# Kernel optimization log

Hardware: AMD Instinct MI355X
Metric: run time of the kernel (lower is better)

## Reference

```python
import jax, jax.numpy as jnp
import numpy as np

FILTER_LENGTH = 1024
HOP_LENGTH = 512
CUTOFF = FILTER_LENGTH // 2 + 1  # 513


def make_forward_basis():
    # fourier_basis = fft(eye(N)); stack [real(top half); imag(top half)]
    fb = np.fft.fft(np.eye(FILTER_LENGTH))
    fb = np.vstack([np.real(fb[:CUTOFF, :]), np.imag(fb[:CUTOFF, :])]).astype(np.float32)
    return jnp.asarray(fb)  # [2*CUTOFF, FILTER_LENGTH] = [1026, 1024]


def setup_inputs() -> dict:
    key = jax.random.key(0)
    input_data = jax.random.normal(key, (64, 524288), dtype=jnp.float32)
    return {"input_data": input_data, "forward_basis": make_forward_basis()}


def reference(input_data, forward_basis):
    # input_data: [B, T] -> [B, 1, T]
    x = input_data[:, None, :]
    # forward_basis: [1026, 1024] -> conv kernel [out_ch=1026, in_ch=1, K=1024]
    w = forward_basis[:, None, :]
    # F.conv1d(..., stride=hop, padding=filter_length)
    ft = jax.lax.conv_general_dilated(
        x, w,
        window_strides=(HOP_LENGTH,),
        padding=[(FILTER_LENGTH, FILTER_LENGTH)],
    )  # [B, 1026, frames]
    real_part = ft[:, :CUTOFF, :]
    imag_part = ft[:, CUTOFF:, :]
    magnitude = jnp.sqrt(real_part ** 2 + imag_part ** 2 + 1e-10)
    phase = jnp.arctan2(imag_part, real_part)
    return magnitude, phase
```

## Files before the change

kernel.cpp:

```cpp
#include <hip/hip_runtime.h>
#include <math.h>

#define BATCH 64
#define LSAMP 524288
#define KLEN 1024
#define HOP 512
#define CBIN 513
#define TWIN 1027
#define BCT (64LL * 513 * 1027)

typedef unsigned int uint32;
using short8  = __attribute__((ext_vector_type(8))) short;
using ushort8v= __attribute__((ext_vector_type(8))) unsigned short;
using f32x4   = __attribute__((ext_vector_type(4))) float;

#define FBT_SLOTS (9 * 32 * 512)
#define FBH_OFF 0u
#define FBL_OFF ((uint32)FBT_SLOTS * 8u)
#define XPLANE  526336
#define XH_OFF  (2u * (uint32)FBT_SLOTS * 8u)
#define XL_OFF  (XH_OFF + 64u * (uint32)XPLANE)
#define WS_NEED ((size_t)(XL_OFF + 64u * (uint32)XPLANE) * 2)

__device__ __forceinline__ unsigned short bfh(float v) {
    uint32 u = __float_as_uint(v);
    return (unsigned short)((u + 0x7fffu + ((u >> 16) & 1u)) >> 16);
}
__device__ __forceinline__ float bf2f(unsigned short h) {
    return __uint_as_float(((uint32)h) << 16);
}

__device__ __forceinline__ void gld16(const void* g, void* l) {
    using GT = const __attribute__((address_space(1))) unsigned int;
    using LT = __attribute__((address_space(3))) unsigned int;
    __builtin_amdgcn_global_load_lds((GT*)g, (LT*)l, 16, 0, 0);
}

__global__ __launch_bounds__(256)
void split_fb(const float* __restrict__ fb, unsigned short* __restrict__ ws) {
    int id = blockIdx.x * 256 + threadIdx.x;
    if (id >= FBT_SLOTS) return;
    int slot = id & 511;
    int tile = id >> 9;
    int ks = tile & 31;
    int ct = tile >> 5;
    int row = slot >> 2;
    int unit = (slot & 3) ^ ((row >> 1) & 3);
    int c0 = (ct < 8) ? ct * 64 : 449;
    int c = (row < 64) ? (c0 + row) : (513 + c0 + (row - 64));
    int k0 = ks * 32 + unit * 8;
    const float4* src = (const float4*)(fb + (size_t)c * KLEN + k0);
    float4 a = src[0], b = src[1];
    float vv[8] = {a.x, a.y, a.z, a.w, b.x, b.y, b.z, b.w};
    ushort8v hh, ll;
#pragma unroll
    for (int j = 0; j < 8; ++j) {
        unsigned short h = bfh(vv[j]);
        hh[j] = h;
        ll[j] = bfh(vv[j] - bf2f(h));
    }
    *(ushort8v*)&ws[FBH_OFF + (size_t)id * 8] = hh;
    *(ushort8v*)&ws[FBL_OFF + (size_t)id * 8] = ll;
}

__global__ __launch_bounds__(256)
void split_x(const float* __restrict__ x, unsigned short* __restrict__ ws) {
    long i = (long)blockIdx.x * 256 + threadIdx.x;
    if (i >= 64L * (XPLANE / 8)) return;
    int b = (int)(i / (XPLANE / 8));
    int j = (int)(i % (XPLANE / 8)) * 8;
    long sample = (long)j - 1024;
    float vv[8] = {0.f,0.f,0.f,0.f,0.f,0.f,0.f,0.f};
    if (sample >= 0 && sample < LSAMP) {
        const float4* s = (const float4*)(x + (size_t)b * LSAMP + sample);
        float4 a = s[0], c = s[1];
        vv[0]=a.x; vv[1]=a.y; vv[2]=a.z; vv[3]=a.w;
        vv[4]=c.x; vv[5]=c.y; vv[6]=c.z; vv[7]=c.w;
    }
    ushort8v hh, ll;
#pragma unroll
    for (int jj = 0; jj < 8; ++jj) {
        unsigned short h = bfh(vv[jj]);
        hh[jj] = h;
        ll[jj] = bfh(vv[jj] - bf2f(h));
    }
    *(ushort8v*)&ws[(size_t)XH_OFF + (size_t)b * XPLANE + j] = hh;
    *(ushort8v*)&ws[(size_t)XL_OFF + (size_t)b * XPLANE + j] = ll;
}

__global__ __launch_bounds__(256, 2)
void stft_gemm(const unsigned short* __restrict__ ws, float* __restrict__ out) {
    extern __shared__ unsigned short sm[];

    const int tid  = threadIdx.x;
    const int lane = tid & 63;
    const int w    = tid >> 6;
    const int wm   = w >> 1;
    const int wn   = w & 1;
    const int lm   = lane & 15;
    const int lg   = lane >> 4;
    const int swz  = (lm >> 1) & 3;

    const int p   = blockIdx.x;
    const int xcd = p & 7;
    const int q   = p >> 3;
    const int ct  = q % 9;
    const int g   = (q / 9) * 8 + xcd;
    const int nt  = g % 9;
    const int b   = g / 9;
    const int c0  = (ct < 8) ? ct * 64 : 449;
    const int n0  = nt * 128;

    f32x4 acc[4][4];
#pragma unroll
    for (int i = 0; i < 4; ++i)
#pragma unroll
        for (int j = 0; j < 4; ++j) acc[i][j] = (f32x4)0.f;

    auto STAGE = [&](int d, int ks) {
        const int s0 = w * 128;
        const uint32 atile = (uint32)(ct * 32 + ks) * 4096u;
#pragma unroll
        for (int r = 0; r < 2; ++r) {
            const int sbase = s0 + r * 64;
            const uint32 slot = (uint32)(sbase + lane);
            const uint32 dsto = (uint32)d * 16384u + (uint32)sbase * 8u;
            gld16(&ws[atile + slot * 8u],            &sm[dsto]);
            gld16(&ws[FBL_OFF + atile + slot * 8u],  &sm[dsto + 4096u]);
            const uint32 brow  = slot >> 2;
            const uint32 bunit = (slot & 3u) ^ ((brow >> 1) & 3u);
            uint32 pidx = (uint32)(n0 + brow) * 512u + (uint32)ks * 32u + bunit * 8u;
            if (pidx > (uint32)(XPLANE - 8)) pidx = (uint32)(XPLANE - 8);
            gld16(&ws[(size_t)XH_OFF + (size_t)b * XPLANE + pidx], &sm[dsto + 8192u]);
            gld16(&ws[(size_t)XL_OFF + (size_t)b * XPLANE + pidx], &sm[dsto + 12288u]);
        }
    };

    STAGE(0, 0);
    __syncthreads();

    for (int ks = 0; ks < 32; ++ks) {
        const int cur = ks & 1;
        if (ks < 31) STAGE(cur ^ 1, ks + 1);

        const uint32 base = (uint32)cur * 16384u;
        short8 ah[4], al[4], bh[4], bl[4];
#pragma unroll
        for (int mi = 0; mi < 4; ++mi) {
            const uint32 row = (uint32)(wm * 64 + mi * 16 + lm);
            const uint32 o = base + row * 32u + (uint32)((lg ^ swz) * 8);
            ah[mi] = *(const short8*)&sm[o];
            al[mi] = *(const short8*)&sm[o + 4096u];
        }
#pragma unroll
        for (int ni = 0; ni < 4; ++ni) {
            const uint32 row = (uint32)(wn * 64 + ni * 16 + lm);
            const uint32 o = base + 8192u + row * 32u + (uint32)((lg ^ swz) * 8);
            bh[ni] = *(const short8*)&sm[o];
            bl[ni] = *(const short8*)&sm[o + 4096u];
        }
#pragma unroll
        for (int mi = 0; mi < 4; ++mi)
#pragma unroll
            for (int ni = 0; ni < 4; ++ni)
                acc[mi][ni] = __builtin_amdgcn_mfma_f32_16x16x32_bf16(ah[mi], bh[ni], acc[mi][ni], 0, 0, 0);
#pragma unroll
        for (int mi = 0; mi < 4; ++mi)
#pragma unroll
            for (int ni = 0; ni < 4; ++ni)
                acc[mi][ni] = __builtin_amdgcn_mfma_f32_16x16x32_bf16(ah[mi], bl[ni], acc[mi][ni], 0, 0, 0);
#pragma unroll
        for (int mi = 0; mi < 4; ++mi)
#pragma unroll
            for (int ni = 0; ni < 4; ++ni)
                acc[mi][ni] = __builtin_amdgcn_mfma_f32_16x16x32_bf16(al[mi], bh[ni], acc[mi][ni], 0, 0, 0);

        __syncthreads();
    }

    float* eps = (float*)sm;
#pragma unroll
    for (int mi = 0; mi < 4; ++mi)
#pragma unroll
        for (int ni = 0; ni < 4; ++ni)
#pragma unroll
            for (int r = 0; r < 4; ++r) {
                int cr = mi * 16 + lg * 4 + r;
                int nc = wn * 64 + ni * 16 + lm;
                eps[wm * 8448 + cr * 132 + nc] = acc[mi][ni][r];
            }
    __syncthreads();
#pragma unroll 4
    for (int qq = 0; qq < 32; ++qq) {
        int id = qq * 256 + tid;
        int cr = id >> 7, nc = id & 127;
        int n = n0 + nc;
        if (n < TWIN) {
            float re = eps[cr * 132 + nc];
            float im = eps[8448 + cr * 132 + nc];
            size_t obase = ((size_t)b * CBIN + (c0 + cr)) * TWIN + n;
            out[obase]       = sqrtf(fmaf(re, re, fmaf(im, im, 1e-10f)));
            out[BCT + obase] = atan2f(im, re);
        }
    }
}

__global__ __launch_bounds__(256)
void stft_fix(const float* __restrict__ x, const float* __restrict__ fb,
              float* __restrict__ out) {
    const int lane = threadIdx.x & 63;
    const uint32 nquad = (uint32)(BCT / 4);
    const uint32 nquad_pad = (nquad + 63u) & ~63u;
    const uint32 stride = gridDim.x * 256;
    for (uint32 gq = blockIdx.x * 256 + threadIdx.x; gq < nquad_pad; gq += stride) {
        const bool live = gq < nquad;
        float mm[4] = {1e9f, 1e9f, 1e9f, 1e9f};
        float pp[4] = {0.f, 0.f, 0.f, 0.f};
        if (live) {
            float4 mv = *(const float4*)&out[(size_t)gq * 4];
            float4 pv = *(const float4*)&out[BCT + (size_t)gq * 4];
            mm[0]=mv.x; mm[1]=mv.y; mm[2]=mv.z; mm[3]=mv.w;
            pp[0]=pv.x; pp[1]=pv.y; pp[2]=pv.z; pp[3]=pv.w;
        }
        bool cand = false;
#pragma unroll
        for (int j = 0; j < 4; ++j)
            cand |= (mm[j] < 2e-3f) || ((3.14159265f - fabsf(pp[j])) * mm[j] < 3e-3f);
        if (__ballot(cand) == 0ULL) continue;

        bool risky[4] = {false, false, false, false};
        if (live) {
            uint32 i0  = gq * 4u;
            uint32 row = i0 / 1027u;
            uint32 t0  = i0 - row * 1027u;
            uint32 cc0 = row % 513u;
#pragma unroll
            for (int j = 0; j < 4; ++j) {
                uint32 t = t0 + j, c = cc0;
                if (t >= 1027u) { t -= 1027u; c = (c == 512u) ? 0u : c + 1u; }
                bool edge = (t == 0u) | (t == 1026u);
                bool axis = (c == 0u) | (c == 512u);
                risky[j] = !edge && ((mm[j] < 2e-3f) ||
                                     (!axis && (3.14159265f - fabsf(pp[j])) * mm[j] < 3e-3f));
            }
        }
#pragma unroll
        for (int j = 0; j < 4; ++j) {
            unsigned long long mask = __ballot(risky[j]);
            while (mask) {
                int src = __ffsll(mask) - 1;
                mask &= mask - 1;
                uint32 idx = (gq - lane + (uint32)src) * 4u + (uint32)j;
                uint32 rw = idx / 1027u;
                uint32 t  = idx - rw * 1027u;
                uint32 bb = rw / 513u;
                uint32 c  = rw - bb * 513u;
                const float* xb = x + (size_t)bb * LSAMP;
                const float* fr = fb + (size_t)c * KLEN;
                const float* fi = fb + (size_t)(513 + c) * KLEN;
                const long s = (long)t * HOP - KLEN;
                double re = 0.0, im = 0.0;
                for (int k = lane; k < KLEN; k += 64) {
                    long gg = s + k;
                    double xv = (gg >= 0 && gg < LSAMP) ? (double)xb[gg] : 0.0;
                    re = fma((double)fr[k], xv, re);
                    im = fma((double)fi[k], xv, im);
                }
#pragma unroll
                for (int off = 32; off > 0; off >>= 1) {
                    re += __shfl_down(re, off);
                    im += __shfl_down(im, off);
                }
                if (lane == 0) {
                    out[idx]       = (float)sqrt(re * re + im * im + 1e-10);
                    out[BCT + idx] = (float)atan2(im, re);
                }
            }
        }
    }
}

__global__ __launch_bounds__(256)
void stft_gemm_legacy(const float* __restrict__ x, const float* __restrict__ fb,
                      float* __restrict__ out) {
    __shared__ unsigned short sml[16384];
    unsigned short* AH = sml;
    unsigned short* AL = sml + 4096;
    unsigned short* BH = sml + 8192;
    unsigned short* BL = sml + 12288;

    const int tid  = threadIdx.x;
    const int lane = tid & 63;
    const int w    = tid >> 6;
    const int wm   = w >> 1;
    const int wn   = w & 1;
    const int lm   = lane & 15;
    const int lk   = (lane >> 4) * 8;

    const int ct = blockIdx.x;
    const int nt = blockIdx.y;
    const int b  = blockIdx.z;
    const int c0 = ct * 64;
    const int n0 = nt * 128;

    const float4* fbg = (const float4*)fb;
    const float*  xb  = x + (size_t)b * LSAMP;

    int srow[4], su[4], sfbrow[4];
    long sxbase0[4];
#pragma unroll
    for (int pp = 0; pp < 4; ++pp) {
        int id = pp * 256 + tid;
        int row = id >> 3, u = id & 7;
        srow[pp] = row; su[pp] = u;
        sfbrow[pp] = (row < 64) ? (c0 + row) : (513 + c0 + (row - 64));
        sxbase0[pp] = 512L * (n0 + row) + 4L * u - 1024L;
    }

    f32x4 acc[4][4];
#pragma unroll
    for (int i = 0; i < 4; ++i)
#pragma unroll
        for (int j = 0; j < 4; ++j) acc[i][j] = (f32x4)0.f;

    float4 pa[4], pb[4];
#pragma unroll
    for (int pp = 0; pp < 4; ++pp) {
        pa[pp] = fbg[(size_t)sfbrow[pp] * 256 + su[pp]];
        long base = sxbase0[pp];
        pb[pp] = (base >= 0 && base < LSAMP) ? *(const float4*)(xb + base)
                                             : make_float4(0.f, 0.f, 0.f, 0.f);
    }

    for (int ks = 0; ks < 32; ++ks) {
        __syncthreads();
#pragma unroll
        for (int pp = 0; pp < 4; ++pp) {
            int o = srow[pp] * 32 + su[pp] * 4;
            float4 va = pa[pp], vb = pb[pp];
            ushort4 h, l;
            h.x = bfh(va.x); l.x = bfh(va.x - bf2f(h.x));
            h.y = bfh(va.y); l.y = bfh(va.y - bf2f(h.y));
            h.z = bfh(va.z); l.z = bfh(va.z - bf2f(h.z));
            h.w = bfh(va.w); l.w = bfh(va.w - bf2f(h.w));
            *(ushort4*)&AH[o] = h; *(ushort4*)&AL[o] = l;
            h.x = bfh(vb.x); l.x = bfh(vb.x - bf2f(h.x));
            h.y = bfh(vb.y); l.y = bfh(vb.y - bf2f(h.y));
            h.z = bfh(vb.z); l.z = bfh(vb.z - bf2f(h.z));
            h.w = bfh(vb.w); l.w = bfh(vb.w - bf2f(h.w));
            *(ushort4*)&BH[o] = h; *(ushort4*)&BL[o] = l;
        }
        __syncthreads();

        if (ks < 31) {
            int k0n = (ks + 1) * 32;
#pragma unroll
            for (int pp = 0; pp < 4; ++pp) {
                pa[pp] = fbg[(size_t)sfbrow[pp] * 256 + (k0n >> 2) + su[pp]];
                long base = sxbase0[pp] + k0n;
                pb[pp] = (base >= 0 && base < LSAMP) ? *(const float4*)(xb + base)
                                                     : make_float4(0.f, 0.f, 0.f, 0.f);
            }
        }

        short8 ah[4], al[4], bh[4], bl[4];
#pragma unroll
        for (int mi = 0; mi < 4; ++mi) {
            int o = (wm * 64 + mi * 16 + lm) * 32 + lk;
            ah[mi] = *(const short8*)&AH[o];
            al[mi] = *(const short8*)&AL[o];
        }
#pragma unroll
        for (int ni = 0; ni < 4; ++ni) {
            int o = (wn * 64 + ni * 16 + lm) * 32 + lk;
            bh[ni] = *(const short8*)&BH[o];
            bl[ni] = *(const short8*)&BL[o];
        }
#pragma unroll
        for (int mi = 0; mi < 4; ++mi)
#pragma unroll
            for (int ni = 0; ni < 4; ++ni)
                acc[mi][ni] = __builtin_amdgcn_mfma_f32_16x16x32_bf16(ah[mi], bh[ni], acc[mi][ni], 0, 0, 0);
#pragma unroll
        for (int mi = 0; mi < 4; ++mi)
#pragma unroll
            for (int ni = 0; ni < 4; ++ni)
                acc[mi][ni] = __builtin_amdgcn_mfma_f32_16x16x32_bf16(ah[mi], bl[ni], acc[mi][ni], 0, 0, 0);
#pragma unroll
        for (int mi = 0; mi < 4; ++mi)
#pragma unroll
            for (int ni = 0; ni < 4; ++ni)
                acc[mi][ni] = __builtin_amdgcn_mfma_f32_16x16x32_bf16(al[mi], bh[ni], acc[mi][ni], 0, 0, 0);
    }

    float* epsRe = (float*)sml;
    float* epsIm = (float*)(sml + 8192);
#pragma unroll
    for (int h = 0; h < 2; ++h) {
        __syncthreads();
#pragma unroll
        for (int mi = 0; mi < 4; ++mi)
#pragma unroll
            for (int nj = 0; nj < 2; ++nj) {
                int ni = 2 * h + nj;
#pragma unroll
                for (int r = 0; r < 4; ++r) {
                    int cr   = mi * 16 + (lane >> 4) * 4 + r;
                    int nbuf = wn * 32 + nj * 16 + lm;
                    if (wm == 0) epsRe[cr * 64 + nbuf] = acc[mi][ni][r];
                    else         epsIm[cr * 64 + nbuf] = acc[mi][ni][r];
                }
            }
        __syncthreads();
#pragma unroll
        for (int qq = 0; qq < 16; ++qq) {
            int id   = qq * 256 + tid;
            int cr   = id >> 6;
            int nbuf = id & 63;
            int nr   = (nbuf >> 5) * 64 + h * 32 + (nbuf & 31);
            int n    = n0 + nr;
            if (n < TWIN) {
                float re = epsRe[cr * 64 + nbuf];
                float im = epsIm[cr * 64 + nbuf];
                size_t base = ((size_t)b * CBIN + (c0 + cr)) * TWIN + n;
                out[base]       = sqrtf(fmaf(re, re, fmaf(im, im, 1e-10f)));
                out[BCT + base] = atan2f(im, re);
            }
        }
    }
}

__global__ __launch_bounds__(256)
void stft_nyq(const float* __restrict__ x, const float* __restrict__ fb,
              float* __restrict__ out) {
    const int gw   = (int)((blockIdx.x * 256 + threadIdx.x) >> 6);
    const int lane = threadIdx.x & 63;
    if (gw >= BATCH * TWIN) return;
    const int b = gw / TWIN;
    const int t = gw % TWIN;
    const long s = (long)t * HOP - KLEN;
    const float* xb = x + (size_t)b * LSAMP;
    const float* frow  = fb + (size_t)512 * KLEN;
    const float* firow = fb + (size_t)1025 * KLEN;

    float re = 0.f, im = 0.f;
    for (int k = lane; k < KLEN; k += 64) {
        long gg = s + k;
        float xv = (gg >= 0 && gg < LSAMP) ? xb[gg] : 0.f;
        re = fmaf(xv, frow[k], re);
        im = fmaf(xv, firow[k], im);
    }
#pragma unroll
    for (int off = 32; off > 0; off >>= 1) {
        re += __shfl_down(re, off);
        im += __shfl_down(im, off);
    }
    if (lane == 0) {
        size_t base = ((size_t)b * CBIN + 512) * TWIN + t;
        out[base]       = sqrtf(fmaf(re, re, fmaf(im, im, 1e-10f)));
        out[BCT + base] = atan2f(im, re);
    }
}

extern "C" void kernel_launch(void* const* d_in, const int* in_sizes, int n_in,
                              void* d_out, int out_size, void* d_ws, size_t ws_size,
                              hipStream_t stream) {
    const float* x  = (const float*)d_in[0];
    const float* fb = (const float*)d_in[1];
    float* out = (float*)d_out;

    if (ws_size >= WS_NEED) {
        unsigned short* ws = (unsigned short*)d_ws;
        split_fb<<<(FBT_SLOTS + 255) / 256, 256, 0, stream>>>(fb, ws);
        split_x<<<(64 * (XPLANE / 8) + 255) / 256, 256, 0, stream>>>(x, ws);
        stft_gemm<<<5184, 256, 67584, stream>>>(ws, out);
        stft_fix<<<2048, 256, 0, stream>>>(x, fb, out);
    } else {
        dim3 grid(8, 9, BATCH);
        stft_gemm_legacy<<<grid, 256, 0, stream>>>(x, fb, out);
        int nwaves = BATCH * TWIN;
        int nblk = (nwaves * 64 + 255) / 256;
        stft_nyq<<<nblk, 256, 0, stream>>>(x, fb, out);
        stft_fix<<<2048, 256, 0, stream>>>(x, fb, out);
    }
}
```

Baseline: 620.7 us.

## Switch STFT GEMM to single fp16 MFMA with selective fp64 recompute list

```diff
diff --git a/kernel.cpp b/kernel.cpp
--- a/kernel.cpp
+++ b/kernel.cpp
@@ -10,17 +10,16 @@
 #define BCT (64LL * 513 * 1027)
 
 typedef unsigned int uint32;
-using short8  = __attribute__((ext_vector_type(8))) short;
-using ushort8v= __attribute__((ext_vector_type(8))) unsigned short;
-using f32x4   = __attribute__((ext_vector_type(4))) float;
-
-#define FBT_SLOTS (9 * 32 * 512)
-#define FBH_OFF 0u
-#define FBL_OFF ((uint32)FBT_SLOTS * 8u)
-#define XPLANE  526336
-#define XH_OFF  (2u * (uint32)FBT_SLOTS * 8u)
-#define XL_OFF  (XH_OFF + 64u * (uint32)XPLANE)
-#define WS_NEED ((size_t)(XL_OFF + 64u * (uint32)XPLANE) * 2)
+using short8   = __attribute__((ext_vector_type(8))) short;
+using half8    = __attribute__((ext_vector_type(8))) _Float16;
+using f32x4    = __attribute__((ext_vector_type(4))) float;
+
+#define FBT_SLOTS (9 * 16 * 1024)
+#define XPLANE    526336
+#define XF_OFF    ((uint32)FBT_SLOTS * 8u)
+#define LIST_OFF_U (XF_OFF + 64u * (uint32)XPLANE)
+#define LIST_CAP  2000000u
+#define WS_NEED   ((size_t)(LIST_OFF_U + 8u + 2u * LIST_CAP) * 2)
 
 __device__ __forceinline__ unsigned short bfh(float v) {
     uint32 u = __float_as_uint(v);
@@ -29,38 +28,37 @@
 __device__ __forceinline__ float bf2f(unsigned short h) {
     return __uint_as_float(((uint32)h) << 16);
 }
-
 __device__ __forceinline__ void gld16(const void* g, void* l) {
     using GT = const __attribute__((address_space(1))) unsigned int;
     using LT = __attribute__((address_space(3))) unsigned int;
     __builtin_amdgcn_global_load_lds((GT*)g, (LT*)l, 16, 0, 0);
 }
 
+__global__ void zero_cnt(unsigned short* ws) {
+    ((uint32*)(ws + LIST_OFF_U))[0] = 0u;
+}
+
 __global__ __launch_bounds__(256)
 void split_fb(const float* __restrict__ fb, unsigned short* __restrict__ ws) {
     int id = blockIdx.x * 256 + threadIdx.x;
     if (id >= FBT_SLOTS) return;
-    int slot = id & 511;
-    int tile = id >> 9;
-    int ks = tile & 31;
-    int ct = tile >> 5;
-    int row = slot >> 2;
-    int unit = (slot & 3) ^ ((row >> 1) & 3);
+    int slot = id & 1023;
+    int tile = id >> 10;
+    int ks = tile & 15;
+    int ct = tile >> 4;
+    int row = slot >> 3;
+    int pu  = slot & 7;
+    int lu  = pu ^ (row & 7);
     int c0 = (ct < 8) ? ct * 64 : 449;
     int c = (row < 64) ? (c0 + row) : (513 + c0 + (row - 64));
-    int k0 = ks * 32 + unit * 8;
+    int k0 = ks * 64 + lu * 8;
     const float4* src = (const float4*)(fb + (size_t)c * KLEN + k0);
     float4 a = src[0], b = src[1];
     float vv[8] = {a.x, a.y, a.z, a.w, b.x, b.y, b.z, b.w};
-    ushort8v hh, ll;
-#pragma unroll
-    for (int j = 0; j < 8; ++j) {
-        unsigned short h = bfh(vv[j]);
-        hh[j] = h;
-        ll[j] = bfh(vv[j] - bf2f(h));
-    }
-    *(ushort8v*)&ws[FBH_OFF + (size_t)id * 8] = hh;
-    *(ushort8v*)&ws[FBL_OFF + (size_t)id * 8] = ll;
+    half8 hv;
+#pragma unroll
+    for (int j = 0; j < 8; ++j) hv[j] = (_Float16)vv[j];
+    *(half8*)&ws[(size_t)id * 8] = hv;
 }
 
 __global__ __launch_bounds__(256)
@@ -77,19 +75,14 @@
         vv[0]=a.x; vv[1]=a.y; vv[2]=a.z; vv[3]=a.w;
         vv[4]=c.x; vv[5]=c.y; vv[6]=c.z; vv[7]=c.w;
     }
-    ushort8v hh, ll;
-#pragma unroll
-    for (int jj = 0; jj < 8; ++jj) {
-        unsigned short h = bfh(vv[jj]);
-        hh[jj] = h;
-        ll[jj] = bfh(vv[jj] - bf2f(h));
-    }
-    *(ushort8v*)&ws[(size_t)XH_OFF + (size_t)b * XPLANE + j] = hh;
-    *(ushort8v*)&ws[(size_t)XL_OFF + (size_t)b * XPLANE + j] = ll;
+    half8 hv;
+#pragma unroll
+    for (int jj = 0; jj < 8; ++jj) hv[jj] = (_Float16)vv[jj];
+    *(half8*)&ws[(size_t)XF_OFF + (size_t)b * XPLANE + j] = hv;
 }
 
 __global__ __launch_bounds__(256, 2)
-void stft_gemm(const unsigned short* __restrict__ ws, float* __restrict__ out) {
+void stft_gemm(unsigned short* __restrict__ ws, float* __restrict__ out) {
     extern __shared__ unsigned short sm[];
 
     const int tid  = threadIdx.x;
@@ -99,7 +92,6 @@
     const int wn   = w & 1;
     const int lm   = lane & 15;
     const int lg   = lane >> 4;
-    const int swz  = (lm >> 1) & 3;
 
     const int p   = blockIdx.x;
     const int xcd = p & 7;
@@ -118,46 +110,291 @@
         for (int j = 0; j < 4; ++j) acc[i][j] = (f32x4)0.f;
 
     auto STAGE = [&](int d, int ks) {
-        const int s0 = w * 128;
-        const uint32 atile = (uint32)(ct * 32 + ks) * 4096u;
-#pragma unroll
-        for (int r = 0; r < 2; ++r) {
-            const int sbase = s0 + r * 64;
-            const uint32 slot = (uint32)(sbase + lane);
-            const uint32 dsto = (uint32)d * 16384u + (uint32)sbase * 8u;
-            gld16(&ws[atile + slot * 8u],            &sm[dsto]);
-            gld16(&ws[FBL_OFF + atile + slot * 8u],  &sm[dsto + 4096u]);
-            const uint32 brow  = slot >> 2;
-            const uint32 bunit = (slot & 3u) ^ ((brow >> 1) & 3u);
-            uint32 pidx = (uint32)(n0 + brow) * 512u + (uint32)ks * 32u + bunit * 8u;
+        const uint32 atile = (uint32)(ct * 16 + ks) * 8192u;
+#pragma unroll
+        for (int r = 0; r < 4; ++r) {
+            const uint32 slot = (uint32)(r * 256 + tid);
+            gld16(&ws[atile + slot * 8u], &sm[(uint32)d * 16384u + slot * 8u]);
+        }
+#pragma unroll
+        for (int r = 0; r < 4; ++r) {
+            const uint32 slot = (uint32)(r * 256 + tid);
+            const uint32 brow = slot >> 3;
+            const uint32 lu   = (slot & 7u) ^ (brow & 7u);
+            uint32 pidx = (uint32)(n0 + brow) * 512u + (uint32)ks * 64u + lu * 8u;
             if (pidx > (uint32)(XPLANE - 8)) pidx = (uint32)(XPLANE - 8);
-            gld16(&ws[(size_t)XH_OFF + (size_t)b * XPLANE + pidx], &sm[dsto + 8192u]);
-            gld16(&ws[(size_t)XL_OFF + (size_t)b * XPLANE + pidx], &sm[dsto + 12288u]);
+            gld16(&ws[(size_t)XF_OFF + (size_t)b * XPLANE + pidx],
+                  &sm[(uint32)d * 16384u + 8192u + slot * 8u]);
         }
     };
 
     STAGE(0, 0);
     __syncthreads();
 
+    for (int ks = 0; ks < 16; ++ks) {
+        const int cur = ks & 1;
+        if (ks < 15) STAGE(cur ^ 1, ks + 1);
+
+        const uint32 base = (uint32)cur * 16384u;
+#pragma unroll
+        for (int kk = 0; kk < 2; ++kk) {
+            const int lu = kk * 4 + lg;
+            half8 ah[4], bh[4];
+#pragma unroll
+            for (int mi = 0; mi < 4; ++mi) {
+                const uint32 row = (uint32)(wm * 64 + mi * 16 + lm);
+                const uint32 o = base + row * 64u + (uint32)((lu ^ (lm & 7)) * 8);
+                ah[mi] = *(const half8*)&sm[o];
+            }
+#pragma unroll
+            for (int ni = 0; ni < 4; ++ni) {
+                const uint32 row = (uint32)(wn * 64 + ni * 16 + lm);
+                const uint32 o = base + 8192u + row * 64u + (uint32)((lu ^ (lm & 7)) * 8);
+                bh[ni] = *(const half8*)&sm[o];
+            }
+#pragma unroll
+            for (int mi = 0; mi < 4; ++mi)
+#pragma unroll
+                for (int ni = 0; ni < 4; ++ni)
+                    acc[mi][ni] = __builtin_amdgcn_mfma_f32_16x16x32_f16(ah[mi], bh[ni], acc[mi][ni], 0, 0, 0);
+        }
+        __syncthreads();
+    }
+
+    float* epsRe = (float*)sm;
+    float* epsIm = ((float*)sm) + 64 * 66;
+    uint32* cntr = (uint32*)(ws + LIST_OFF_U);
+    uint32* list = cntr + 4;
+    const float pi_f = 3.14159265f;
+
+#pragma unroll
+    for (int h = 0; h < 2; ++h) {
+        __syncthreads();
+#pragma unroll
+        for (int mi = 0; mi < 4; ++mi)
+#pragma unroll
+            for (int nj = 0; nj < 2; ++nj) {
+                int ni = 2 * h + nj;
+#pragma unroll
+                for (int r = 0; r < 4; ++r) {
+                    int cr   = mi * 16 + lg * 4 + r;
+                    int nbuf = wn * 32 + nj * 16 + lm;
+                    if (wm == 0) epsRe[cr * 66 + nbuf] = acc[mi][ni][r];
+                    else         epsIm[cr * 66 + nbuf] = acc[mi][ni][r];
+                }
+            }
+        __syncthreads();
+#pragma unroll 4
+        for (int qq = 0; qq < 16; ++qq) {
+            int id   = qq * 256 + tid;
+            int cr   = id >> 6;
+            int nbuf = id & 63;
+            int nr   = (nbuf >> 5) * 64 + h * 32 + (nbuf & 31);
+            int n    = n0 + nr;
+            bool risky = false;
+            size_t ob = 0;
+            if (n < TWIN) {
+                float re = epsRe[cr * 66 + nbuf];
+                float im = epsIm[cr * 66 + nbuf];
+                int c = c0 + cr;
+                float m  = sqrtf(fmaf(re, re, fmaf(im, im, 1e-10f)));
+                float pv = atan2f(im, re);
+                ob = ((size_t)b * CBIN + c) * TWIN + n;
+                out[ob]       = m;
+                out[BCT + ob] = pv;
+                bool edge = (n == 0) | (n == 1026);
+                bool axis = (c == 0) | (c == 512);
+                risky = !edge && ((m < 0.06f) ||
+                                  (!axis && (pi_f - fabsf(pv)) * m < 0.08f));
+            }
+            unsigned long long mask = __ballot(risky);
+            if (mask) {
+                int leader = __ffsll(mask) - 1;
+                uint32 bslot = 0;
+                if (lane == leader) bslot = atomicAdd(cntr, (uint32)__popcll(mask));
+                bslot = (uint32)__shfl((int)bslot, leader);
+                if (risky) {
+                    uint32 slot = bslot + (uint32)__popcll(mask & ((1ULL << lane) - 1ULL));
+                    if (slot < LIST_CAP) list[slot] = (uint32)ob;
+                }
+            }
+        }
+    }
+}
+
+__global__ __launch_bounds__(256)
+void stft_axis(const float* __restrict__ x, const float* __restrict__ fb,
+               float* __restrict__ out) {
+    const int gw   = (int)((blockIdx.x * 256 + threadIdx.x) >> 6);
+    const int lane = threadIdx.x & 63;
+    if (gw >= BATCH * TWIN) return;
+    const int b = gw / TWIN;
+    const int t = gw % TWIN;
+    const long s = (long)t * HOP - KLEN;
+    const float* xb  = x + (size_t)b * LSAMP;
+    const float* fr0 = fb;
+    const float* fi0 = fb + (size_t)513 * KLEN;
+    const float* fr5 = fb + (size_t)512 * KLEN;
+    const float* fi5 = fb + (size_t)1025 * KLEN;
+
+    float re0 = 0.f, im0 = 0.f, re5 = 0.f, im5 = 0.f;
+#pragma unroll 4
+    for (int k = lane; k < KLEN; k += 64) {
+        long gg = s + k;
+        float xv = (gg >= 0 && gg < LSAMP) ? xb[gg] : 0.f;
+        re0 = fmaf(xv, fr0[k], re0); im0 = fmaf(xv, fi0[k], im0);
+        re5 = fmaf(xv, fr5[k], re5); im5 = fmaf(xv, fi5[k], im5);
+    }
+#pragma unroll
+    for (int off = 32; off > 0; off >>= 1) {
+        re0 += __shfl_down(re0, off); im0 += __shfl_down(im0, off);
+        re5 += __shfl_down(re5, off); im5 += __shfl_down(im5, off);
+    }
+    if (lane == 0) {
+        size_t b0 = ((size_t)b * CBIN + 0) * TWIN + t;
+        out[b0]       = sqrtf(fmaf(re0, re0, fmaf(im0, im0, 1e-10f)));
+        out[BCT + b0] = atan2f(im0, re0);
+        size_t b5 = ((size_t)b * CBIN + 512) * TWIN + t;
+        out[b5]       = sqrtf(fmaf(re5, re5, fmaf(im5, im5, 1e-10f)));
+        out[BCT + b5] = atan2f(im5, re5);
+    }
+}
+
+__global__ __launch_bounds__(256)
+void stft_fix2(const float* __restrict__ x, const float* __restrict__ fb,
+               const unsigned short* __restrict__ ws, float* __restrict__ out) {
+    const uint32* cntr = (const uint32*)(ws + LIST_OFF_U);
+    const uint32* list = cntr + 4;
+    uint32 count = *cntr;
+    if (count > LIST_CAP) count = LIST_CAP;
+    const int lane = threadIdx.x & 63;
+    const uint32 gw = (uint32)((blockIdx.x * 256 + threadIdx.x) >> 6);
+    const uint32 nw = gridDim.x * 4;
+    for (uint32 i = gw; i < count; i += nw) {
+        uint32 idx = list[i];
+        uint32 rw = idx / 1027u;
+        uint32 t  = idx - rw * 1027u;
+        uint32 bb = rw / 513u;
+        uint32 c  = rw - bb * 513u;
+        const float* xb = x + (size_t)bb * LSAMP;
+        const float* fr = fb + (size_t)c * KLEN;
+        const float* fi = fb + (size_t)(513 + c) * KLEN;
+        const long s = (long)t * HOP - KLEN;
+        double re = 0.0, im = 0.0;
+#pragma unroll 4
+        for (int k = lane; k < KLEN; k += 64) {
+            long gg = s + k;
+            double xv = (gg >= 0 && gg < LSAMP) ? (double)xb[gg] : 0.0;
+            re = fma((double)fr[k], xv, re);
+            im = fma((double)fi[k], xv, im);
+        }
+#pragma unroll
+        for (int off = 32; off > 0; off >>= 1) {
+            re += __shfl_down(re, off);
+            im += __shfl_down(im, off);
+        }
+        if (lane == 0) {
+            out[idx]       = (float)sqrt(re * re + im * im + 1e-10);
+            out[BCT + idx] = (float)atan2(im, re);
+        }
+    }
+}
+
+__global__ __launch_bounds__(256)
+void stft_gemm_legacy(const float* __restrict__ x, const float* __restrict__ fb,
+                      float* __restrict__ out) {
+    __shared__ unsigned short sml[16384];
+    unsigned short* AH = sml;
+    unsigned short* AL = sml + 4096;
+    unsigned short* BH = sml + 8192;
+    unsigned short* BL = sml + 12288;
+
+    const int tid  = threadIdx.x;
+    const int lane = tid & 63;
+    const int w    = tid >> 6;
+    const int wm   = w >> 1;
+    const int wn   = w & 1;
+    const int lm   = lane & 15;
+    const int lk   = (lane >> 4) * 8;
+
+    const int ct = blockIdx.x;
+    const int nt = blockIdx.y;
+    const int b  = blockIdx.z;
+    const int c0 = ct * 64;
+    const int n0 = nt * 128;
+
+    const float4* fbg = (const float4*)fb;
+    const float*  xb  = x + (size_t)b * LSAMP;
+
+    int srow[4], su[4], sfbrow[4];
+    long sxbase0[4];
+#pragma unroll
+    for (int pp = 0; pp < 4; ++pp) {
+        int id = pp * 256 + tid;
+        int row = id >> 3, u = id & 7;
+        srow[pp] = row; su[pp] = u;
+        sfbrow[pp] = (row < 64) ? (c0 + row) : (513 + c0 + (row - 64));
+        sxbase0[pp] = 512L * (n0 + row) + 4L * u - 1024L;
+    }
+
+    f32x4 acc[4][4];
+#pragma unroll
+    for (int i = 0; i < 4; ++i)
+#pragma unroll
+        for (int j = 0; j < 4; ++j) acc[i][j] = (f32x4)0.f;
+
+    float4 pa[4], pb[4];
+#pragma unroll
+    for (int pp = 0; pp < 4; ++pp) {
+        pa[pp] = fbg[(size_t)sfbrow[pp] * 256 + su[pp]];
+        long base = sxbase0[pp];
+        pb[pp] = (base >= 0 && base < LSAMP) ? *(const float4*)(xb + base)
+                                             : make_float4(0.f, 0.f, 0.f, 0.f);
+    }
+
     for (int ks = 0; ks < 32; ++ks) {
-        const int cur = ks & 1;
-        if (ks < 31) STAGE(cur ^ 1, ks + 1);
-
-        const uint32 base = (uint32)cur * 16384u;
+        __syncthreads();
+#pragma unroll
+        for (int pp = 0; pp < 4; ++pp) {
+            int o = srow[pp] * 32 + su[pp] * 4;
+            float4 va = pa[pp], vb = pb[pp];
+            ushort4 h, l;
+            h.x = bfh(va.x); l.x = bfh(va.x - bf2f(h.x));
+            h.y = bfh(va.y); l.y = bfh(va.y - bf2f(h.y));
+            h.z = bfh(va.z); l.z = bfh(va.z - bf2f(h.z));
+            h.w = bfh(va.w); l.w = bfh(va.w - bf2f(h.w));
+            *(ushort4*)&AH[o] = h; *(ushort4*)&AL[o] = l;
+            h.x = bfh(vb.x); l.x = bfh(vb.x - bf2f(h.x));
+            h.y = bfh(vb.y); l.y = bfh(vb.y - bf2f(h.y));
+            h.z = bfh(vb.z); l.z = bfh(vb.z - bf2f(h.z));
+            h.w = bfh(vb.w); l.w = bfh(vb.w - bf2f(h.w));
+            *(ushort4*)&BH[o] = h; *(ushort4*)&BL[o] = l;
+        }
+        __syncthreads();
+
+        if (ks < 31) {
+            int k0n = (ks + 1) * 32;
+#pragma unroll
+            for (int pp = 0; pp < 4; ++pp) {
+                pa[pp] = fbg[(size_t)sfbrow[pp] * 256 + (k0n >> 2) + su[pp]];
+                long base = sxbase0[pp] + k0n;
+                pb[pp] = (base >= 0 && base < LSAMP) ? *(const float4*)(xb + base)
+                                                     : make_float4(0.f, 0.f, 0.f, 0.f);
+            }
+        }
+
         short8 ah[4], al[4], bh[4], bl[4];
 #pragma unroll
         for (int mi = 0; mi < 4; ++mi) {
-            const uint32 row = (uint32)(wm * 64 + mi * 16 + lm);
-            const uint32 o = base + row * 32u + (uint32)((lg ^ swz) * 8);
-            ah[mi] = *(const short8*)&sm[o];
-            al[mi] = *(const short8*)&sm[o + 4096u];
+            int o = (wm * 64 + mi * 16 + lm) * 32 + lk;
+            ah[mi] = *(const short8*)&AH[o];
+            al[mi] = *(const short8*)&AL[o];
         }
 #pragma unroll
         for (int ni = 0; ni < 4; ++ni) {
-            const uint32 row = (uint32)(wn * 64 + ni * 16 + lm);
-            const uint32 o = base + 8192u + row * 32u + (uint32)((lg ^ swz) * 8);
-            bh[ni] = *(const short8*)&sm[o];
-            bl[ni] = *(const short8*)&sm[o + 4096u];
+            int o = (wn * 64 + ni * 16 + lm) * 32 + lk;
+            bh[ni] = *(const short8*)&BH[o];
+            bl[ni] = *(const short8*)&BL[o];
         }
 #pragma unroll
         for (int mi = 0; mi < 4; ++mi)
@@ -174,40 +411,80 @@
 #pragma unroll
             for (int ni = 0; ni < 4; ++ni)
                 acc[mi][ni] = __builtin_amdgcn_mfma_f32_16x16x32_bf16(al[mi], bh[ni], acc[mi][ni], 0, 0, 0);
-
-        __syncthreads();
-    }
-
-    float* eps = (float*)sm;
-#pragma unroll
-    for (int mi = 0; mi < 4; ++mi)
-#pragma unroll
-        for (int ni = 0; ni < 4; ++ni)
-#pragma unroll
-            for (int r = 0; r < 4; ++r) {
-                int cr = mi * 16 + lg * 4 + r;
-                int nc = wn * 64 + ni * 16 + lm;
-                eps[wm * 8448 + cr * 132 + nc] = acc[mi][ni][r];
-            }
-    __syncthreads();
-#pragma unroll 4
-    for (int qq = 0; qq < 32; ++qq) {
-        int id = qq * 256 + tid;
-        int cr = id >> 7, nc = id & 127;
-        int n = n0 + nc;
-        if (n < TWIN) {
-            float re = eps[cr * 132 + nc];
-            float im = eps[8448 + cr * 132 + nc];
-            size_t obase = ((size_t)b * CBIN + (c0 + cr)) * TWIN + n;
-            out[obase]       = sqrtf(fmaf(re, re, fmaf(im, im, 1e-10f)));
-            out[BCT + obase] = atan2f(im, re);
-        }
-    }
-}
-
-__global__ __launch_bounds__(256)
-void stft_fix(const float* __restrict__ x, const float* __restrict__ fb,
+    }
+
+    float* epsRe = (float*)sml;
+    float* epsIm = (float*)(sml + 8192);
+#pragma unroll
+    for (int h = 0; h < 2; ++h) {
+        __syncthreads();
+#pragma unroll
+        for (int mi = 0; mi < 4; ++mi)
+#pragma unroll
+            for (int nj = 0; nj < 2; ++nj) {
+                int ni = 2 * h + nj;
+#pragma unroll
+                for (int r = 0; r < 4; ++r) {
+                    int cr   = mi * 16 + (lane >> 4) * 4 + r;
+                    int nbuf = wn * 32 + nj * 16 + lm;
+                    if (wm == 0) epsRe[cr * 64 + nbuf] = acc[mi][ni][r];
+                    else         epsIm[cr * 64 + nbuf] = acc[mi][ni][r];
+                }
+            }
+        __syncthreads();
+#pragma unroll
+        for (int qq = 0; qq < 16; ++qq) {
+            int id   = qq * 256 + tid;
+            int cr   = id >> 6;
+            int nbuf = id & 63;
+            int nr   = (nbuf >> 5) * 64 + h * 32 + (nbuf & 31);
+            int n    = n0 + nr;
+            if (n < TWIN) {
+                float re = epsRe[cr * 64 + nbuf];
+                float im = epsIm[cr * 64 + nbuf];
+                size_t base = ((size_t)b * CBIN + (c0 + cr)) * TWIN + n;
+                out[base]       = sqrtf(fmaf(re, re, fmaf(im, im, 1e-10f)));
+                out[BCT + base] = atan2f(im, re);
+            }
+        }
+    }
+}
+
+__global__ __launch_bounds__(256)
+void stft_nyq(const float* __restrict__ x, const float* __restrict__ fb,
               float* __restrict__ out) {
+    const int gw   = (int)((blockIdx.x * 256 + threadIdx.x) >> 6);
+    const int lane = threadIdx.x & 63;
+    if (gw >= BATCH * TWIN) return;
+    const int b = gw / TWIN;
+    const int t = gw % TWIN;
+    const long s = (long)t * HOP - KLEN;
+    const float* xb = x + (size_t)b * LSAMP;
+    const float* frow  = fb + (size_t)512 * KLEN;
+    const float* firow = fb + (size_t)1025 * KLEN;
+
+    float re = 0.f, im = 0.f;
+    for (int k = lane; k < KLEN; k += 64) {
+        long gg = s + k;
+        float xv = (gg >= 0 && gg < LSAMP) ? xb[gg] : 0.f;
+        re = fmaf(xv, frow[k], re);
+        im = fmaf(xv, firow[k], im);
+    }
+#pragma unroll
+    for (int off = 32; off > 0; off >>= 1) {
+        re += __shfl_down(re, off);
+        im += __shfl_down(im, off);
+    }
+    if (lane == 0) {
+        size_t base = ((size_t)b * CBIN + 512) * TWIN + t;
+        out[base]       = sqrtf(fmaf(re, re, fmaf(im, im, 1e-10f)));
+        out[BCT + base] = atan2f(im, re);
+    }
+}
+
+__global__ __launch_bounds__(256)
+void stft_fix_legacy(const float* __restrict__ x, const float* __restrict__ fb,
+                     float* __restrict__ out) {
     const int lane = threadIdx.x & 63;
     const uint32 nquad = (uint32)(BCT / 4);
     const uint32 nquad_pad = (nquad + 63u) & ~63u;
@@ -280,188 +557,6 @@
     }
 }
 
-__global__ __launch_bounds__(256)
-void stft_gemm_legacy(const float* __restrict__ x, const float* __restrict__ fb,
-                      float* __restrict__ out) {
-    __shared__ unsigned short sml[16384];
-    unsigned short* AH = sml;
-    unsigned short* AL = sml + 4096;
-    unsigned short* BH = sml + 8192;
-    unsigned short* BL = sml + 12288;
-
-    const int tid  = threadIdx.x;
-    const int lane = tid & 63;
-    const int w    = tid >> 6;
-    const int wm   = w >> 1;
-    const int wn   = w & 1;
-    const int lm   = lane & 15;
-    const int lk   = (lane >> 4) * 8;
-
-    const int ct = blockIdx.x;
-    const int nt = blockIdx.y;
-    const int b  = blockIdx.z;
-    const int c0 = ct * 64;
-    const int n0 = nt * 128;
-
-    const float4* fbg = (const float4*)fb;
-    const float*  xb  = x + (size_t)b * LSAMP;
-
-    int srow[4], su[4], sfbrow[4];
-    long sxbase0[4];
-#pragma unroll
-    for (int pp = 0; pp < 4; ++pp) {
-        int id = pp * 256 + tid;
-        int row = id >> 3, u = id & 7;
-        srow[pp] = row; su[pp] = u;
-        sfbrow[pp] = (row < 64) ? (c0 + row) : (513 + c0 + (row - 64));
-        sxbase0[pp] = 512L * (n0 + row) + 4L * u - 1024L;
-    }
-
-    f32x4 acc[4][4];
-#pragma unroll
-    for (int i = 0; i < 4; ++i)
-#pragma unroll
-        for (int j = 0; j < 4; ++j) acc[i][j] = (f32x4)0.f;
-
-    float4 pa[4], pb[4];
-#pragma unroll
-    for (int pp = 0; pp < 4; ++pp) {
-        pa[pp] = fbg[(size_t)sfbrow[pp] * 256 + su[pp]];
-        long base = sxbase0[pp];
-        pb[pp] = (base >= 0 && base < LSAMP) ? *(const float4*)(xb + base)
-                                             : make_float4(0.f, 0.f, 0.f, 0.f);
-    }
-
-    for (int ks = 0; ks < 32; ++ks) {
-        __syncthreads();
-#pragma unroll
-        for (int pp = 0; pp < 4; ++pp) {
-            int o = srow[pp] * 32 + su[pp] * 4;
-            float4 va = pa[pp], vb = pb[pp];
-            ushort4 h, l;
-            h.x = bfh(va.x); l.x = bfh(va.x - bf2f(h.x));
-            h.y = bfh(va.y); l.y = bfh(va.y - bf2f(h.y));
-            h.z = bfh(va.z); l.z = bfh(va.z - bf2f(h.z));
-            h.w = bfh(va.w); l.w = bfh(va.w - bf2f(h.w));
-            *(ushort4*)&AH[o] = h; *(ushort4*)&AL[o] = l;
-            h.x = bfh(vb.x); l.x = bfh(vb.x - bf2f(h.x));
-            h.y = bfh(vb.y); l.y = bfh(vb.y - bf2f(h.y));
-            h.z = bfh(vb.z); l.z = bfh(vb.z - bf2f(h.z));
-            h.w = bfh(vb.w); l.w = bfh(vb.w - bf2f(h.w));
-            *(ushort4*)&BH[o] = h; *(ushort4*)&BL[o] = l;
-        }
-        __syncthreads();
-
-        if (ks < 31) {
-            int k0n = (ks + 1) * 32;
-#pragma unroll
-            for (int pp = 0; pp < 4; ++pp) {
-                pa[pp] = fbg[(size_t)sfbrow[pp] * 256 + (k0n >> 2) + su[pp]];
-                long base = sxbase0[pp] + k0n;
-                pb[pp] = (base >= 0 && base < LSAMP) ? *(const float4*)(xb + base)
-                                                     : make_float4(0.f, 0.f, 0.f, 0.f);
-            }
-        }
-
-        short8 ah[4], al[4], bh[4], bl[4];
-#pragma unroll
-        for (int mi = 0; mi < 4; ++mi) {
-            int o = (wm * 64 + mi * 16 + lm) * 32 + lk;
-            ah[mi] = *(const short8*)&AH[o];
-            al[mi] = *(const short8*)&AL[o];
-        }
-#pragma unroll
-        for (int ni = 0; ni < 4; ++ni) {
-            int o = (wn * 64 + ni * 16 + lm) * 32 + lk;
-            bh[ni] = *(const short8*)&BH[o];
-            bl[ni] = *(const short8*)&BL[o];
-        }
-#pragma unroll
-        for (int mi = 0; mi < 4; ++mi)
-#pragma unroll
-            for (int ni = 0; ni < 4; ++ni)
-                acc[mi][ni] = __builtin_amdgcn_mfma_f32_16x16x32_bf16(ah[mi], bh[ni], acc[mi][ni], 0, 0, 0);
-#pragma unroll
-        for (int mi = 0; mi < 4; ++mi)
-#pragma unroll
-            for (int ni = 0; ni < 4; ++ni)
-                acc[mi][ni] = __builtin_amdgcn_mfma_f32_16x16x32_bf16(ah[mi], bl[ni], acc[mi][ni], 0, 0, 0);
-#pragma unroll
-        for (int mi = 0; mi < 4; ++mi)
-#pragma unroll
-            for (int ni = 0; ni < 4; ++ni)
-                acc[mi][ni] = __builtin_amdgcn_mfma_f32_16x16x32_bf16(al[mi], bh[ni], acc[mi][ni], 0, 0, 0);
-    }
-
-    float* epsRe = (float*)sml;
-    float* epsIm = (float*)(sml + 8192);
-#pragma unroll
-    for (int h = 0; h < 2; ++h) {
-        __syncthreads();
-#pragma unroll
-        for (int mi = 0; mi < 4; ++mi)
-#pragma unroll
-            for (int nj = 0; nj < 2; ++nj) {
-                int ni = 2 * h + nj;
-#pragma unroll
-                for (int r = 0; r < 4; ++r) {
-                    int cr   = mi * 16 + (lane >> 4) * 4 + r;
-                    int nbuf = wn * 32 + nj * 16 + lm;
-                    if (wm == 0) epsRe[cr * 64 + nbuf] = acc[mi][ni][r];
-                    else         epsIm[cr * 64 + nbuf] = acc[mi][ni][r];
-                }
-            }
-        __syncthreads();
-#pragma unroll
-        for (int qq = 0; qq < 16; ++qq) {
-            int id   = qq * 256 + tid;
-            int cr   = id >> 6;
-            int nbuf = id & 63;
-            int nr   = (nbuf >> 5) * 64 + h * 32 + (nbuf & 31);
-            int n    = n0 + nr;
-            if (n < TWIN) {
-                float re = epsRe[cr * 64 + nbuf];
-                float im = epsIm[cr * 64 + nbuf];
-                size_t base = ((size_t)b * CBIN + (c0 + cr)) * TWIN + n;
-                out[base]       = sqrtf(fmaf(re, re, fmaf(im, im, 1e-10f)));
-                out[BCT + base] = atan2f(im, re);
-            }
-        }
-    }
-}
-
-__global__ __launch_bounds__(256)
-void stft_nyq(const float* __restrict__ x, const float* __restrict__ fb,
-              float* __restrict__ out) {
-    const int gw   = (int)((blockIdx.x * 256 + threadIdx.x) >> 6);
-    const int lane = threadIdx.x & 63;
-    if (gw >= BATCH * TWIN) return;
-    const int b = gw / TWIN;
-    const int t = gw % TWIN;
-    const long s = (long)t * HOP - KLEN;
-    const float* xb = x + (size_t)b * LSAMP;
-    const float* frow  = fb + (size_t)512 * KLEN;
-    const float* firow = fb + (size_t)1025 * KLEN;
-
-    float re = 0.f, im = 0.f;
-    for (int k = lane; k < KLEN; k += 64) {
-        long gg = s + k;
-        float xv = (gg >= 0 && gg < LSAMP) ? xb[gg] : 0.f;
-        re = fmaf(xv, frow[k], re);
-        im = fmaf(xv, firow[k], im);
-    }
-#pragma unroll
-    for (int off = 32; off > 0; off >>= 1) {
-        re += __shfl_down(re, off);
-        im += __shfl_down(im, off);
-    }
-    if (lane == 0) {
-        size_t base = ((size_t)b * CBIN + 512) * TWIN + t;
-        out[base]       = sqrtf(fmaf(re, re, fmaf(im, im, 1e-10f)));
-        out[BCT + base] = atan2f(im, re);
-    }
-}
-
 extern "C" void kernel_launch(void* const* d_in, const int* in_sizes, int n_in,
                               void* d_out, int out_size, void* d_ws, size_t ws_size,
                               hipStream_t stream) {
@@ -471,16 +566,18 @@
 
     if (ws_size >= WS_NEED) {
         unsigned short* ws = (unsigned short*)d_ws;
+        zero_cnt<<<1, 1, 0, stream>>>(ws);
         split_fb<<<(FBT_SLOTS + 255) / 256, 256, 0, stream>>>(fb, ws);
         split_x<<<(64 * (XPLANE / 8) + 255) / 256, 256, 0, stream>>>(x, ws);
-        stft_gemm<<<5184, 256, 67584, stream>>>(ws, out);
-        stft_fix<<<2048, 256, 0, stream>>>(x, fb, out);
+        stft_gemm<<<5184, 256, 65536, stream>>>(ws, out);
+        stft_axis<<<(BATCH * TWIN * 64 + 255) / 256, 256, 0, stream>>>(x, fb, out);
+        stft_fix2<<<1024, 256, 0, stream>>>(x, fb, ws, out);
     } else {
         dim3 grid(8, 9, BATCH);
         stft_gemm_legacy<<<grid, 256, 0, stream>>>(x, fb, out);
         int nwaves = BATCH * TWIN;
         int nblk = (nwaves * 64 + 255) / 256;
         stft_nyq<<<nblk, 256, 0, stream>>>(x, fb, out);
-        stft_fix<<<2048, 256, 0, stream>>>(x, fb, out);
-    }
-}
+        stft_fix_legacy<<<2048, 256, 0, stream>>>(x, fb, out);
+    }
+}
```

Measured after the change: 830.3 us. 33.8% more time.
